# Kernel tuning notes

Hardware: AMD Instinct MI355X
Metric: run time of the kernel (lower is better)

## Reference

```python
import jax, jax.numpy as jnp
import numpy as np

B, C, H, W = 16, 512, 32, 32
HID = 4 * C


def setup_inputs() -> dict:
    key = jax.random.key(0)
    k_x, k_w1, k_w2 = jax.random.split(key, 3)
    x = jax.random.normal(k_x, (B, C, H, W), dtype=jnp.float32)
    # 1x1 conv weights stored as [out, in] matrices (kernel_size=1)
    w1 = jax.random.normal(k_w1, (HID, C), dtype=jnp.float32) * (1.0 / np.sqrt(C))
    b1 = jnp.zeros((HID,), dtype=jnp.float32)
    w2 = jax.random.normal(k_w2, (C, HID), dtype=jnp.float32) * (1.0 / np.sqrt(HID))
    b2 = jnp.zeros((C,), dtype=jnp.float32)
    return {"x": x, "w1": w1, "b1": b1, "w2": w2, "b2": b2}


def reference(x, w1, b1, w2, b2):
    Bd, Cd, Hd, Wd = x.shape
    scale = Cd ** (-0.5)
    xf = x.reshape(Bd, Cd, Hd * Wd)          # [B, C, N]
    q = jnp.swapaxes(xf, -1, -2)              # [B, N, C]
    # full spatial self-attention: scores [B, N, N]
    attn = jax.nn.softmax(jnp.einsum('bnc,bcm->bnm', q, xf) * scale, axis=-1)
    out = jnp.einsum('bnm,bmc->bnc', attn, q)  # [B, N, C]
    # 1x1-conv FFN applied per spatial position
    h = jax.nn.relu(jnp.einsum('bnc,dc->bnd', out, w1) + b1)   # [B, N, 4C]
    y = jnp.einsum('bnd,cd->bnc', h, w2) + b2                  # [B, N, C]
    y = jnp.swapaxes(y, -1, -2).reshape(Bd, Cd, Hd, Wd)
    return y + x
```

## Files before the change

kernel.cpp:

```cpp
#include <hip/hip_runtime.h>

#define BATCH 16
#define CH    512
#define NSP   1024
#define HIDD  2048

typedef __bf16 bf16x8 __attribute__((ext_vector_type(8)));
typedef float floatx4 __attribute__((ext_vector_type(4)));

__device__ __forceinline__ float bf2f(unsigned short u) {
    union { unsigned int i; float f; } v; v.i = ((unsigned int)u) << 16; return v.f;
}
__device__ __forceinline__ unsigned short f2bf(float f) {
    union { float f; unsigned int i; } v; v.f = f;
    unsigned int i = v.i;
    return (unsigned short)((i + 0x7FFFu + ((i >> 16) & 1u)) >> 16);
}

__device__ __forceinline__ void gload16(const void* g, void* l) {
    __builtin_amdgcn_global_load_lds(
        (__attribute__((address_space(1))) unsigned int*)(g),
        (__attribute__((address_space(3))) unsigned int*)(l),
        16, 0, 0);
}
#define MEMFENCE asm volatile("" ::: "memory")

template<int EPI, int MAP, int DEPTH>
__global__ __launch_bounds__(256, (DEPTH == 2) ? 3 : 2)
void gemm_bt(const unsigned short* __restrict__ A,
             const unsigned short* __restrict__ Bm,
             void* __restrict__ Cout,
             int Nn, int K,
             long sAb, long sBb, long sCb,
             const float* __restrict__ bias, float scale,
             const float* __restrict__ resid,
             float* __restrict__ aux)
{
    constexpr int NBUF = DEPTH + 1;
    __shared__ unsigned short sA[NBUF][128 * 32];
    __shared__ unsigned short sB[NBUF][128 * 32];
    __shared__ float sInv[128];

    const int tid  = threadIdx.x;
    const int lane = tid & 63;
    const int w    = tid >> 6;
    const int quad = lane >> 4;
    const int l15  = lane & 15;
    const int mw   = (w >> 1) * 64;
    const int nw   = (w & 1) * 64;

    const int F = blockIdx.x;
    int m0, n0, b;
    if constexpr (MAP == 1) {
        const int xcd = F & 7, s = F >> 3;
        b = xcd + ((s >> 5) << 3);
        const int j = s & 31; m0 = (j >> 2) << 7; n0 = (j & 3) << 7;
    } else if constexpr (MAP == 3) {
        const int xcd = F & 7, s = F >> 3;
        b = 0; m0 = (s & 3) << 7; n0 = ((xcd << 4) + (s >> 2)) << 7;
    } else {
        const int xcd = F & 7; int s = F >> 3;
        b = xcd + ((s >= 36) ? 8 : 0);
        if (s >= 36) s -= 36;
        int tm = 0;
        while (s >= 8 - tm) { s -= 8 - tm; tm++; }
        m0 = tm << 7; n0 = (tm + s) << 7;
    }

    if constexpr (EPI == 6) {
        if (tid < 128) {
            const float* p = aux + (size_t)b * NSP * 16
                           + (size_t)(m0 + tid) * 16;
            float s = 0.f;
#pragma unroll
            for (int k = 0; k < 16; k++) s += p[k];
            sInv[tid] = 1.0f / s;
        }
        MEMFENCE;
    }

    A  += (size_t)b * sAb;
    Bm += (size_t)b * sBb;

    const int srow = lane >> 2;
    const int sg   = (lane & 3) ^ ((lane >> 3) & 3);
    const unsigned short* pA = A  + (size_t)(m0 + w * 32 + srow) * K + sg * 8;
    const unsigned short* pB = Bm + (size_t)(n0 + w * 32 + srow) * K + sg * 8;
    const size_t rowskip16 = (size_t)16 * K;
    const int woff = w * 1024;
    const int rslot = ((l15 >> 1) & 3);

    floatx4 acc[4][4];
#pragma unroll
    for (int i = 0; i < 4; i++)
#pragma unroll
        for (int j = 0; j < 4; j++) acc[i][j] = (floatx4){0.f, 0.f, 0.f, 0.f};

    const int nIter = K >> 5;
    const int kLast = K - 32;

#pragma unroll
    for (int d = 0; d < DEPTH; ++d) {
        unsigned short* dA = &sA[d][0] + woff;
        unsigned short* dB = &sB[d][0] + woff;
        gload16(pA + d * 32,             dA);
        gload16(pA + d * 32 + rowskip16, dA + 512);
        gload16(pB + d * 32,             dB);
        gload16(pB + d * 32 + rowskip16, dB + 512);
        MEMFENCE;
    }

    int bcur = 0, bpf = DEPTH;
    for (int it = 0; it < nIter; ++it) {
        if constexpr (DEPTH == 2)
            asm volatile("s_waitcnt vmcnt(4)\n\ts_barrier" ::: "memory");
        else
            asm volatile("s_waitcnt vmcnt(8)\n\ts_barrier" ::: "memory");

        const int kpf = (it + DEPTH) * 32 <= kLast ? (it + DEPTH) * 32 : kLast;
        unsigned short* dA = &sA[0][0] + bpf * 4096 + woff;
        unsigned short* dB = &sB[0][0] + bpf * 4096 + woff;
        gload16(pA + kpf,             dA);
        gload16(pA + kpf + rowskip16, dA + 512);
        gload16(pB + kpf,             dB);
        gload16(pB + kpf + rowskip16, dB + 512);
        MEMFENCE;

        const unsigned short* bufA = &sA[0][0] + bcur * 4096;
        const unsigned short* bufB = &sB[0][0] + bcur * 4096;
        bf16x8 af[4], bfr[4];
#pragma unroll
        for (int mi = 0; mi < 4; mi++)
            af[mi] = *(const bf16x8*)(bufA + (mw + mi * 16 + l15) * 32
                                      + (quad ^ rslot) * 8);
#pragma unroll
        for (int ni = 0; ni < 4; ni++)
            bfr[ni] = *(const bf16x8*)(bufB + (nw + ni * 16 + l15) * 32
                                       + (quad ^ rslot) * 8);
#pragma unroll
        for (int mi = 0; mi < 4; mi++)
#pragma unroll
            for (int ni = 0; ni < 4; ni++)
                acc[mi][ni] = __builtin_amdgcn_mfma_f32_16x16x32_bf16(
                    af[mi], bfr[ni], acc[mi][ni], 0, 0, 0);

        bcur = bcur == NBUF - 1 ? 0 : bcur + 1;
        bpf  = bpf  == NBUF - 1 ? 0 : bpf  + 1;
    }
    asm volatile("s_waitcnt vmcnt(0)" ::: "memory");

    if constexpr (EPI == 4) {
        float* Of = (float*)Cout;
#pragma unroll
        for (int mi = 0; mi < 4; mi++) {
#pragma unroll
            for (int r = 0; r < 4; r++) {
                const int c = m0 + mw + mi * 16 + quad * 4 + r;
                const float bv = bias[c];
#pragma unroll
                for (int ni = 0; ni < 4; ni++) {
                    const int j  = n0 + nw + ni * 16 + l15;
                    const int bb = j >> 10, ns = j & 1023;
                    const size_t a = (size_t)bb * CH * NSP + (size_t)c * NSP + ns;
                    Of[a] = acc[mi][ni][r] + bv + resid[a];
                }
            }
        }
    } else if constexpr (EPI == 5) {
#pragma unroll
        for (int mi = 0; mi < 4; mi++)
#pragma unroll
            for (int ni = 0; ni < 4; ni++)
#pragma unroll
                for (int r = 0; r < 4; r++)
                    acc[mi][ni][r] = __expf(acc[mi][ni][r] * scale);
        {
            const int chunk = (n0 + nw) >> 6;
            float* ps = aux + (size_t)b * NSP * 16;
#pragma unroll
            for (int mi = 0; mi < 4; mi++) {
#pragma unroll
                for (int r = 0; r < 4; r++) {
                    float s = acc[mi][0][r] + acc[mi][1][r]
                            + acc[mi][2][r] + acc[mi][3][r];
                    s += __shfl_xor(s, 1);
                    s += __shfl_xor(s, 2);
                    s += __shfl_xor(s, 4);
                    s += __shfl_xor(s, 8);
                    if (l15 == 0)
                        ps[(size_t)(m0 + mw + mi * 16 + quad * 4 + r) * 16
                           + chunk] = s;
                }
            }
        }
        unsigned short* Cb = (unsigned short*)Cout + (size_t)b * sCb;
#pragma unroll
        for (int mi = 0; mi < 4; mi++) {
#pragma unroll
            for (int r = 0; r < 4; r++) {
                const size_t rowoff =
                    (size_t)(m0 + mw + mi * 16 + quad * 4 + r) * Nn;
#pragma unroll
                for (int ni = 0; ni < 4; ni++)
                    Cb[rowoff + n0 + nw + ni * 16 + l15] =
                        f2bf(acc[mi][ni][r]);
            }
        }
        if constexpr (MAP == 4) {
            if (m0 != n0) {
                const int chunkt = (m0 + mw) >> 6;
                float* ps = aux + (size_t)b * NSP * 16;
#pragma unroll
                for (int ni = 0; ni < 4; ni++) {
                    float s = 0.f;
#pragma unroll
                    for (int mi = 0; mi < 4; mi++)
#pragma unroll
                        for (int r = 0; r < 4; r++) s += acc[mi][ni][r];
                    s += __shfl_xor(s, 16);
                    s += __shfl_xor(s, 32);
                    if (quad == 0)
                        ps[(size_t)(n0 + nw + ni * 16 + l15) * 16 + chunkt] = s;
                }
#pragma unroll
                for (int ni = 0; ni < 4; ni++) {
                    const size_t rowoff =
                        (size_t)(n0 + nw + ni * 16 + l15) * Nn;
#pragma unroll
                    for (int mi = 0; mi < 4; mi++) {
                        ushort4 v;
                        v.x = f2bf(acc[mi][ni][0]);
                        v.y = f2bf(acc[mi][ni][1]);
                        v.z = f2bf(acc[mi][ni][2]);
                        v.w = f2bf(acc[mi][ni][3]);
                        *(ushort4*)(Cb + rowoff + m0 + mw + mi * 16 + quad * 4)
                            = v;
                    }
                }
            }
        }
    } else {
        __syncthreads();
        unsigned short* Cb = (unsigned short*)Cout + (size_t)b * sCb;
#pragma unroll
        for (int mi = 0; mi < 4; mi++) {
#pragma unroll
            for (int r = 0; r < 4; r++) {
                const int lrow = mw + mi * 16 + quad * 4 + r;
                const float iv = sInv[lrow];
                const size_t rowoff = (size_t)(m0 + lrow) * Nn;
#pragma unroll
                for (int ni = 0; ni < 4; ni++)
                    Cb[rowoff + n0 + nw + ni * 16 + l15] =
                        f2bf(acc[mi][ni][r] * iv);
            }
        }
    }
}

__global__ __launch_bounds__(256, 4)
void gemm_final_n64(const unsigned short* __restrict__ A,
                    const unsigned short* __restrict__ Bm,
                    float* __restrict__ Of,
                    const float* __restrict__ bias,
                    const float* __restrict__ resid)
{
    const int K = HIDD;
    __shared__ unsigned short sA[3][128 * 32];
    __shared__ unsigned short sB[3][64 * 32];

    const int tid  = threadIdx.x;
    const int lane = tid & 63;
    const int w    = tid >> 6;
    const int quad = lane >> 4;
    const int l15  = lane & 15;
    const int mw   = w * 32;

    const int F = blockIdx.x;
    const int xcd = F & 7, s = F >> 3;
    const int m0 = (s & 3) << 7;
    const int n0 = ((xcd << 5) + (s >> 2)) << 6;

    const int srow = lane >> 2;
    const int sg   = (lane & 3) ^ ((lane >> 3) & 3);
    const unsigned short* pA = A  + (size_t)(m0 + w * 32 + srow) * K + sg * 8;
    const unsigned short* pB = Bm + (size_t)(n0 + w * 16 + srow) * K + sg * 8;
    const size_t rowskip16 = (size_t)16 * K;
    const int woffA = w * 1024;
    const int woffB = w * 512;
    const int rslot = ((l15 >> 1) & 3);

    floatx4 acc[2][4];
#pragma unroll
    for (int i = 0; i < 2; i++)
#pragma unroll
        for (int j = 0; j < 4; j++) acc[i][j] = (floatx4){0.f, 0.f, 0.f, 0.f};

    const int nIter = K >> 5;
    const int kLast = K - 32;

#pragma unroll
    for (int d = 0; d < 2; ++d) {
        unsigned short* dA = &sA[d][0] + woffA;
        unsigned short* dB = &sB[d][0] + woffB;
        gload16(pA + d * 32,             dA);
        gload16(pA + d * 32 + rowskip16, dA + 512);
        gload16(pB + d * 32,             dB);
        MEMFENCE;
    }

    int bcur = 0, bpf = 2;
    for (int it = 0; it < nIter; ++it) {
        asm volatile("s_waitcnt vmcnt(3)\n\ts_barrier" ::: "memory");

        const int kpf = (it + 2) * 32 <= kLast ? (it + 2) * 32 : kLast;
        unsigned short* dA = &sA[bpf][0] + woffA;
        unsigned short* dB = &sB[bpf][0] + woffB;
        gload16(pA + kpf,             dA);
        gload16(pA + kpf + rowskip16, dA + 512);
        gload16(pB + kpf,             dB);
        MEMFENCE;

        const unsigned short* bufA = &sA[bcur][0];
        const unsigned short* bufB = &sB[bcur][0];
        bf16x8 af[2], bfr[4];
#pragma unroll
        for (int mi = 0; mi < 2; mi++)
            af[mi] = *(const bf16x8*)(bufA + (mw + mi * 16 + l15) * 32
                                      + (quad ^ rslot) * 8);
#pragma unroll
        for (int ni = 0; ni < 4; ni++)
            bfr[ni] = *(const bf16x8*)(bufB + (ni * 16 + l15) * 32
                                       + (quad ^ rslot) * 8);
#pragma unroll
        for (int mi = 0; mi < 2; mi++)
#pragma unroll
            for (int ni = 0; ni < 4; ni++)
                acc[mi][ni] = __builtin_amdgcn_mfma_f32_16x16x32_bf16(
                    af[mi], bfr[ni], acc[mi][ni], 0, 0, 0);

        bcur = bcur == 2 ? 0 : bcur + 1;
        bpf  = bpf  == 2 ? 0 : bpf  + 1;
    }
    asm volatile("s_waitcnt vmcnt(0)" ::: "memory");

#pragma unroll
    for (int mi = 0; mi < 2; mi++) {
#pragma unroll
        for (int r = 0; r < 4; r++) {
            const int c = m0 + mw + mi * 16 + quad * 4 + r;
            const float bv = bias[c];
#pragma unroll
            for (int ni = 0; ni < 4; ni++) {
                const int j  = n0 + ni * 16 + l15;
                const int bb = j >> 10, ns = j & 1023;
                const size_t a = (size_t)bb * CH * NSP + (size_t)c * NSP + ns;
                Of[a] = acc[mi][ni][r] + bv + resid[a];
            }
        }
    }
}

__global__ __launch_bounds__(256, 2)
void ffn1_wide(const unsigned short* __restrict__ A,
               const unsigned short* __restrict__ Bm,
               unsigned short* __restrict__ Cout,
               const float* __restrict__ bias)
{
    const int K = CH, Nn = HIDD;
    __shared__ unsigned short sA[3][128 * 32];
    __shared__ unsigned short sB[3][256 * 32];

    const int tid  = threadIdx.x;
    const int lane = tid & 63;
    const int w    = tid >> 6;
    const int quad = lane >> 4;
    const int l15  = lane & 15;
    const int mw   = (w >> 1) * 64;
    const int nw   = (w & 1) * 128;

    const int F = blockIdx.x;
    const int xcd = F & 7, s = F >> 3;
    const int m0 = ((xcd << 4) + (s >> 3)) << 7;
    const int n0 = (s & 7) << 8;

    const int srow = lane >> 2;
    const int sg   = (lane & 3) ^ ((lane >> 3) & 3);
    const unsigned short* pA = A  + (size_t)(m0 + w * 32 + srow) * K + sg * 8;
    const unsigned short* pB = Bm + (size_t)(n0 + w * 64 + srow) * K + sg * 8;
    const size_t rowskip16 = (size_t)16 * K;
    const int woffA = w * 1024;
    const int woffB = w * 2048;
    const int rslot = ((l15 >> 1) & 3);

    floatx4 acc[4][8];
#pragma unroll
    for (int i = 0; i < 4; i++)
#pragma unroll
        for (int j = 0; j < 8; j++) acc[i][j] = (floatx4){0.f, 0.f, 0.f, 0.f};

    const int nIter = K >> 5;
    const int kLast = K - 32;

#pragma unroll
    for (int d = 0; d < 2; ++d) {
        unsigned short* dA = &sA[d][0] + woffA;
        unsigned short* dB = &sB[d][0] + woffB;
        gload16(pA + d * 32,                 dA);
        gload16(pA + d * 32 +     rowskip16, dA + 512);
        gload16(pB + d * 32,                 dB);
        gload16(pB + d * 32 +     rowskip16, dB + 512);
        gload16(pB + d * 32 + 2 * rowskip16, dB + 1024);
        gload16(pB + d * 32 + 3 * rowskip16, dB + 1536);
        MEMFENCE;
    }

    int bcur = 0, bpf = 2;
    for (int it = 0; it < nIter; ++it) {
        asm volatile("s_waitcnt vmcnt(6)\n\ts_barrier" ::: "memory");

        const int kpf = (it + 2) * 32 <= kLast ? (it + 2) * 32 : kLast;
        unsigned short* dA = &sA[0][0] + bpf * 4096 + woffA;
        unsigned short* dB = &sB[0][0] + bpf * 8192 + woffB;
        gload16(pA + kpf,                 dA);
        gload16(pA + kpf +     rowskip16, dA + 512);
        gload16(pB + kpf,                 dB);
        gload16(pB + kpf +     rowskip16, dB + 512);
        gload16(pB + kpf + 2 * rowskip16, dB + 1024);
        gload16(pB + kpf + 3 * rowskip16, dB + 1536);
        MEMFENCE;

        const unsigned short* bufA = &sA[0][0] + bcur * 4096;
        const unsigned short* bufB = &sB[0][0] + bcur * 8192;
        bf16x8 af[4], bfr[8];
#pragma unroll
        for (int mi = 0; mi < 4; mi++)
            af[mi] = *(const bf16x8*)(bufA + (mw + mi * 16 + l15) * 32
                                      + (quad ^ rslot) * 8);
#pragma unroll
        for (int ni = 0; ni < 8; ni++)
            bfr[ni] = *(const bf16x8*)(bufB + (nw + ni * 16 + l15) * 32
                                       + (quad ^ rslot) * 8);
#pragma unroll
        for (int mi = 0; mi < 4; mi++)
#pragma unroll
            for (int ni = 0; ni < 8; ni++)
                acc[mi][ni] = __builtin_amdgcn_mfma_f32_16x16x32_bf16(
                    af[mi], bfr[ni], acc[mi][ni], 0, 0, 0);

        bcur = bcur == 2 ? 0 : bcur + 1;
        bpf  = bpf  == 2 ? 0 : bpf  + 1;
    }
    asm volatile("s_waitcnt vmcnt(0)" ::: "memory");

    float bv[8];
#pragma unroll
    for (int ni = 0; ni < 8; ni++) bv[ni] = bias[n0 + nw + ni * 16 + l15];
#pragma unroll
    for (int mi = 0; mi < 4; mi++) {
#pragma unroll
        for (int r = 0; r < 4; r++) {
            const size_t rowoff =
                (size_t)(m0 + mw + mi * 16 + quad * 4 + r) * Nn;
#pragma unroll
            for (int ni = 0; ni < 8; ni++)
                Cout[rowoff + n0 + nw + ni * 16 + l15] =
                    f2bf(fmaxf(acc[mi][ni][r] + bv[ni], 0.f));
        }
    }
}

__global__ __launch_bounds__(256)
void prep_kernel(const float* __restrict__ x,
                 unsigned short* __restrict__ Xbf,
                 unsigned short* __restrict__ XT,
                 const float* __restrict__ w1,
                 unsigned short* __restrict__ W1b,
                 const float* __restrict__ w2,
                 unsigned short* __restrict__ W2b)
{
    const int tx = threadIdx.x, ty = threadIdx.y;
    const int z = blockIdx.z;
    if (z < 16) {
        __shared__ float tile[32][33];
        const int n0 = blockIdx.x * 32, c0 = blockIdx.y * 32, b = z;
        const size_t base = (size_t)b * CH * NSP;
#pragma unroll
        for (int i = ty; i < 32; i += 8) {
            float v = x[base + (size_t)(c0 + i) * NSP + n0 + tx];
            tile[i][tx] = v;
            Xbf[base + (size_t)(c0 + i) * NSP + n0 + tx] = f2bf(v);
        }
        __syncthreads();
        const size_t tbase = (size_t)b * NSP * CH;
#pragma unroll
        for (int i = ty; i < 32; i += 8)
            XT[tbase + (size_t)(n0 + i) * CH + c0 + tx] = f2bf(tile[tx][i]);
    } else {
        const int tid = ty * 32 + tx;
        const int blk = (z - 16) * 512 + blockIdx.y * 32 + blockIdx.x;
        const int i = blk * 256 + tid;
        if (i < HIDD * CH) W1b[i] = f2bf(w1[i]);
        else               W2b[i - HIDD * CH] = f2bf(w2[i - HIDD * CH]);
    }
}

extern "C" void kernel_launch(void* const* d_in, const int* in_sizes, int n_in,
                              void* d_out, int out_size, void* d_ws, size_t ws_size,
                              hipStream_t stream)
{
    const float* x  = (const float*)d_in[0];
    const float* w1 = (const float*)d_in[1];
    const float* b1 = (const float*)d_in[2];
    const float* w2 = (const float*)d_in[3];
    const float* b2 = (const float*)d_in[4];
    float* out = (float*)d_out;

    char* ws = (char*)d_ws;
    unsigned short* Xbf = (unsigned short*)ws; ws += (size_t)BATCH * CH * NSP * 2;
    unsigned short* XT  = (unsigned short*)ws; ws += (size_t)BATCH * NSP * CH * 2;
    unsigned short* W1b = (unsigned short*)ws; ws += (size_t)HIDD * CH * 2;
    unsigned short* W2b = (unsigned short*)ws; ws += (size_t)CH * HIDD * 2;
    unsigned short* P   = (unsigned short*)ws; ws += (size_t)BATCH * NSP * NSP * 2;
    unsigned short* O   = (unsigned short*)ws; ws += (size_t)BATCH * NSP * CH * 2;
    unsigned short* Hb  = (unsigned short*)ws; ws += (size_t)BATCH * NSP * HIDD * 2;
    float*          Ps  = (float*)ws;          ws += (size_t)BATCH * NSP * 16 * 4;

    const dim3 blk(256);

    prep_kernel<<<dim3(32, 16, 32), dim3(32, 8), 0, stream>>>(
        x, Xbf, XT, w1, W1b, w2, W2b);

    gemm_bt<5, 4, 2><<<dim3(576), blk, 0, stream>>>(
        XT, XT, P, NSP, CH,
        (long)NSP * CH, (long)NSP * CH, (long)NSP * NSP, nullptr,
        0.04419417382415922f, nullptr, Ps);

    gemm_bt<6, 1, 2><<<dim3(512), blk, 0, stream>>>(
        P, Xbf, O, CH, NSP,
        (long)NSP * NSP, (long)CH * NSP, (long)NSP * CH, nullptr, 1.f,
        nullptr, Ps);

    ffn1_wide<<<dim3(1024), blk, 0, stream>>>(O, W1b, Hb, b1);

    gemm_final_n64<<<dim3(1024), blk, 0, stream>>>(
        W2b, Hb, out, b2, x);
}
```

Before: 256.6 us.

## Enlarge final FFN GEMM tile to 128x128 with four-stage, two-step-unrolled pipeline

The final W2 GEMM moves from 128x64 tiles with a 3-buffer pipeline to 128x128 tiles. Each wave now computes a 64x64 sub-tile with a 4x4 MFMA accumulator. The K loop processes two 32-wide slices per barrier using 4 LDS buffers, with prefetches issued after a second barrier. This is meant to raise arithmetic intensity per LDS/global load and halve barrier count. The cost is half as many blocks, lower occupancy (launch bound 2), and more LDS and registers per block.

Result: faster. 242.5 us (-5.5%).

```diff
diff --git a/kernel.cpp b/kernel.cpp
--- a/kernel.cpp
+++ b/kernel.cpp
@@ -258,101 +258,109 @@
     }
 }
 
-__global__ __launch_bounds__(256, 4)
-void gemm_final_n64(const unsigned short* __restrict__ A,
-                    const unsigned short* __restrict__ Bm,
-                    float* __restrict__ Of,
-                    const float* __restrict__ bias,
-                    const float* __restrict__ resid)
+__global__ __launch_bounds__(256, 2)
+void gemm_final_u2(const unsigned short* __restrict__ A,
+                   const unsigned short* __restrict__ Bm,
+                   float* __restrict__ Of,
+                   const float* __restrict__ bias,
+                   const float* __restrict__ resid)
 {
     const int K = HIDD;
-    __shared__ unsigned short sA[3][128 * 32];
-    __shared__ unsigned short sB[3][64 * 32];
+    __shared__ unsigned short sA[4][128 * 32];
+    __shared__ unsigned short sB[4][128 * 32];
 
     const int tid  = threadIdx.x;
     const int lane = tid & 63;
     const int w    = tid >> 6;
     const int quad = lane >> 4;
     const int l15  = lane & 15;
-    const int mw   = w * 32;
+    const int mw   = (w >> 1) * 64;
+    const int nw   = (w & 1) * 64;
 
     const int F = blockIdx.x;
     const int xcd = F & 7, s = F >> 3;
     const int m0 = (s & 3) << 7;
-    const int n0 = ((xcd << 5) + (s >> 2)) << 6;
+    const int n0 = ((xcd << 4) + (s >> 2)) << 7;
 
     const int srow = lane >> 2;
     const int sg   = (lane & 3) ^ ((lane >> 3) & 3);
     const unsigned short* pA = A  + (size_t)(m0 + w * 32 + srow) * K + sg * 8;
-    const unsigned short* pB = Bm + (size_t)(n0 + w * 16 + srow) * K + sg * 8;
+    const unsigned short* pB = Bm + (size_t)(n0 + w * 32 + srow) * K + sg * 8;
     const size_t rowskip16 = (size_t)16 * K;
-    const int woffA = w * 1024;
-    const int woffB = w * 512;
+    const int woff = w * 1024;
     const int rslot = ((l15 >> 1) & 3);
 
-    floatx4 acc[2][4];
-#pragma unroll
-    for (int i = 0; i < 2; i++)
+    floatx4 acc[4][4];
+#pragma unroll
+    for (int i = 0; i < 4; i++)
 #pragma unroll
         for (int j = 0; j < 4; j++) acc[i][j] = (floatx4){0.f, 0.f, 0.f, 0.f};
 
-    const int nIter = K >> 5;
     const int kLast = K - 32;
 
 #pragma unroll
-    for (int d = 0; d < 2; ++d) {
-        unsigned short* dA = &sA[d][0] + woffA;
-        unsigned short* dB = &sB[d][0] + woffB;
+    for (int d = 0; d < 4; ++d) {
+        unsigned short* dA = &sA[d][0] + woff;
+        unsigned short* dB = &sB[d][0] + woff;
         gload16(pA + d * 32,             dA);
         gload16(pA + d * 32 + rowskip16, dA + 512);
         gload16(pB + d * 32,             dB);
+        gload16(pB + d * 32 + rowskip16, dB + 512);
         MEMFENCE;
     }
 
-    int bcur = 0, bpf = 2;
-    for (int it = 0; it < nIter; ++it) {
-        asm volatile("s_waitcnt vmcnt(3)\n\ts_barrier" ::: "memory");
-
-        const int kpf = (it + 2) * 32 <= kLast ? (it + 2) * 32 : kLast;
-        unsigned short* dA = &sA[bpf][0] + woffA;
-        unsigned short* dB = &sB[bpf][0] + woffB;
-        gload16(pA + kpf,             dA);
-        gload16(pA + kpf + rowskip16, dA + 512);
-        gload16(pB + kpf,             dB);
-        MEMFENCE;
-
-        const unsigned short* bufA = &sA[bcur][0];
-        const unsigned short* bufB = &sB[bcur][0];
-        bf16x8 af[2], bfr[4];
-#pragma unroll
-        for (int mi = 0; mi < 2; mi++)
-            af[mi] = *(const bf16x8*)(bufA + (mw + mi * 16 + l15) * 32
-                                      + (quad ^ rslot) * 8);
-#pragma unroll
-        for (int ni = 0; ni < 4; ni++)
-            bfr[ni] = *(const bf16x8*)(bufB + (ni * 16 + l15) * 32
-                                       + (quad ^ rslot) * 8);
-#pragma unroll
-        for (int mi = 0; mi < 2; mi++)
+    const int nBody = K >> 6;
+    for (int i = 0; i < nBody; ++i) {
+        asm volatile("s_waitcnt vmcnt(8)\n\ts_barrier" ::: "memory");
+
+#pragma unroll
+        for (int t = 0; t < 2; ++t) {
+            const int buf = (2 * i + t) & 3;
+            const unsigned short* bufA = &sA[buf][0];
+            const unsigned short* bufB = &sB[buf][0];
+            bf16x8 af[4], bfr[4];
+#pragma unroll
+            for (int mi = 0; mi < 4; mi++)
+                af[mi] = *(const bf16x8*)(bufA + (mw + mi * 16 + l15) * 32
+                                          + (quad ^ rslot) * 8);
 #pragma unroll
             for (int ni = 0; ni < 4; ni++)
-                acc[mi][ni] = __builtin_amdgcn_mfma_f32_16x16x32_bf16(
-                    af[mi], bfr[ni], acc[mi][ni], 0, 0, 0);
-
-        bcur = bcur == 2 ? 0 : bcur + 1;
-        bpf  = bpf  == 2 ? 0 : bpf  + 1;
+                bfr[ni] = *(const bf16x8*)(bufB + (nw + ni * 16 + l15) * 32
+                                           + (quad ^ rslot) * 8);
+#pragma unroll
+            for (int mi = 0; mi < 4; mi++)
+#pragma unroll
+                for (int ni = 0; ni < 4; ni++)
+                    acc[mi][ni] = __builtin_amdgcn_mfma_f32_16x16x32_bf16(
+                        af[mi], bfr[ni], acc[mi][ni], 0, 0, 0);
+        }
+
+        __builtin_amdgcn_s_barrier();
+#pragma unroll
+        for (int t = 0; t < 2; ++t) {
+            const int kt = 2 * i + 4 + t;
+            const int kpf = (kt * 32 <= kLast) ? kt * 32 : kLast;
+            const int buf = kt & 3;
+            unsigned short* dA = &sA[buf][0] + woff;
+            unsigned short* dB = &sB[buf][0] + woff;
+            gload16(pA + kpf,             dA);
+            gload16(pA + kpf + rowskip16, dA + 512);
+            gload16(pB + kpf,             dB);
+            gload16(pB + kpf + rowskip16, dB + 512);
+            MEMFENCE;
+        }
     }
     asm volatile("s_waitcnt vmcnt(0)" ::: "memory");
 
 #pragma unroll
-    for (int mi = 0; mi < 2; mi++) {
+    for (int mi = 0; mi < 4; mi++) {
 #pragma unroll
         for (int r = 0; r < 4; r++) {
             const int c = m0 + mw + mi * 16 + quad * 4 + r;
             const float bv = bias[c];
 #pragma unroll
             for (int ni = 0; ni < 4; ni++) {
-                const int j  = n0 + ni * 16 + l15;
+                const int j  = n0 + nw + ni * 16 + l15;
                 const int bb = j >> 10, ns = j & 1023;
                 const size_t a = (size_t)bb * CH * NSP + (size_t)c * NSP + ns;
                 Of[a] = acc[mi][ni][r] + bv + resid[a];
@@ -543,6 +551,6 @@
 
     ffn1_wide<<<dim3(1024), blk, 0, stream>>>(O, W1b, Hb, b1);
 
-    gemm_final_n64<<<dim3(1024), blk, 0, stream>>>(
+    gemm_final_u2<<<dim3(512), blk, 0, stream>>>(
         W2b, Hb, out, b2, x);
 }
```
